# Optimization experiments

Hardware: AMD Instinct MI355X
Metric: run time of the kernel (lower is better)

Reference implementation:

```python
import jax, jax.numpy as jnp
import numpy as np

G = 8          # GroupNorm groups
EPS = 1e-5
L = 4          # num_layers
C = 64         # hidden_channels
CIN = 2        # in_channels


def group_norm(x, gamma, beta):
    B, Cc, H, W = x.shape
    xr = x.reshape(B, G, Cc // G, H, W)
    mu = xr.mean(axis=(2, 3, 4), keepdims=True)
    var = xr.var(axis=(2, 3, 4), keepdims=True)
    xn = ((xr - mu) * jax.lax.rsqrt(var + EPS)).reshape(B, Cc, H, W)
    return xn * gamma[:, None, None] + beta[:, None, None]


def conv1x1(x, w, b):
    # x: [B,Ci,H,W], w: [Co,Ci] -> [B,Co,H,W]
    return jnp.einsum('bchw,oc->bohw', x, w) + b[None, :, None, None]


def conv3x3(x, w, b):
    y = jax.lax.conv_general_dilated(x, w, (1, 1), 'SAME',
                                     dimension_numbers=('NCHW', 'OIHW', 'NCHW'))
    return y + b[None, :, None, None]


def setup_inputs() -> dict:
    key = jax.random.key(0)
    ks = jax.random.split(key, 20)
    s = 0.05
    inp = {
        'x': jax.random.normal(ks[0], (2, CIN, 256, 256), jnp.float32),
        'hidden': jnp.zeros((2, L, C, C), jnp.float32),
        'W_in': jax.random.normal(ks[1], (C, CIN, 3, 3), jnp.float32) * s,
        'b_in': jnp.zeros((C,), jnp.float32),
        'gamma': jnp.ones((L, C), jnp.float32),
        'beta': jnp.zeros((L, C), jnp.float32),
        'Wq': jax.random.normal(ks[2], (L, C, C), jnp.float32) * s,
        'bq': jnp.zeros((L, C), jnp.float32),
        'Wk': jax.random.normal(ks[3], (L, C, C), jnp.float32) * s,
        'bk': jnp.zeros((L, C), jnp.float32),
        'Wv': jax.random.normal(ks[4], (L, C, C), jnp.float32) * s,
        'bv': jnp.zeros((L, C), jnp.float32),
        'Wg': jax.random.normal(ks[5], (L, 2 * C, C), jnp.float32) * s,
        'bg': jnp.zeros((L, 2 * C), jnp.float32),
        'Wp': jax.random.normal(ks[6], (L, C, C), jnp.float32) * s,
        'bp': jnp.zeros((L, C), jnp.float32),
        'W_out': jax.random.normal(ks[7], (CIN, C, 3, 3), jnp.float32) * s,
        'b_out': jnp.zeros((CIN,), jnp.float32),
    }
    return inp


def gla_layer(feat, prev_mem, gamma, beta, Wq, bq, Wk, bk, Wv, bv, Wg, bg, Wp, bp):
    B, Cc, H, W = feat.shape
    N = H * W
    scale = Cc ** (-0.5)
    xn = group_norm(feat, gamma, beta)
    q = conv1x1(xn, Wq, bq).reshape(B, Cc, N) * scale
    k = conv1x1(xn, Wk, bk).reshape(B, Cc, N)
    v = conv1x1(xn, Wv, bv).reshape(B, Cc, N)
    gates = conv1x1(xn, Wg, bg).reshape(B, 2 * Cc, N)
    f_gate = jax.nn.sigmoid(gates[:, :Cc])
    i_gate = jax.nn.sigmoid(gates[:, Cc:])
    k_gated = k * i_gate
    new_knowledge = jnp.einsum('bcn,bdn->bcd', k_gated, v) / N  # [B,C,C]
    global_forget = f_gate.mean(axis=2)[:, :, None]              # [B,C,1]
    new_mem = global_forget * prev_mem + new_knowledge
    retrieved = jnp.einsum('bcn,bcd->bdn', q, new_mem).reshape(B, Cc, H, W)
    out = conv1x1(retrieved, Wp, bp) + feat
    return out, new_mem


def reference(x, hidden, W_in, b_in, gamma, beta, Wq, bq, Wk, bk, Wv, bv,
              Wg, bg, Wp, bp, W_out, b_out):
    feat = conv3x3(x, W_in, b_in)
    mems = []
    for i in range(L):
        feat, m = gla_layer(feat, hidden[:, i], gamma[i], beta[i],
                            Wq[i], bq[i], Wk[i], bk[i], Wv[i], bv[i],
                            Wg[i], bg[i], Wp[i], bp[i])
        mems.append(m)
    new_hidden = jnp.stack(mems, axis=1)  # [B,L,C,C]
    out = conv3x3(feat, W_out, b_out) + x
    return out, new_hidden
```

## Files before the change

kernel.cpp:

```cpp
#include <hip/hip_runtime.h>
#include <hip/hip_bf16.h>

typedef __hip_bfloat16 bf16;
typedef __attribute__((ext_vector_type(8))) short bf16x8;
typedef __attribute__((ext_vector_type(4))) short short4v;
typedef __attribute__((ext_vector_type(4))) float f32x4;

#define BATCH 2
#define CH 64
#define NPIX 65536
#define HDIM 256
#define NLAYER 4
#define NGRP 8
#define NSLOT 512

#define OFS_FEAT   0ull
#define OFS_KSLOT  16777216ull
#define OFS_MEMBG  25165824ull
#define OFS_FSUM   25182208ull
#define OFS_SSUM   25198592ull
#define OFS_BEFF   25214976ull
#define OFS_MEFFB  25215488ull
#define OFS_WKB    25231872ull
#define OFS_WVB    25264640ull
#define OFS_WGB    25297408ull
#define OFS_WTOUT  25362944ull
#define OFS_WPB    25367552ull
#define OFS_WQTB   25400320ull
#define ZERO_BYTES 32768

__device__ __forceinline__ float sigmoidf_(float x){ return 1.0f/(1.0f+__expf(-x)); }

__device__ __forceinline__ short f2bs(float x){
  unsigned u = __float_as_uint(x);
  u += 0x7fffu + ((u >> 16) & 1u);
  return (short)(u >> 16);
}
__device__ __forceinline__ float bs2f(short x){
  return __uint_as_float(((unsigned)(unsigned short)x) << 16);
}

__device__ __forceinline__ float waveReduce(float v){
  #pragma unroll
  for (int off=32; off; off>>=1) v += __shfl_xor(v, off, 64);
  return v;
}

__global__ void k_prepw(const float* __restrict__ Wk, const float* __restrict__ Wv,
                        const float* __restrict__ Wg, const float* __restrict__ Wout,
                        const float* __restrict__ Wp, const float* __restrict__ Wq,
                        short* __restrict__ Wkb, short* __restrict__ Wvb,
                        short* __restrict__ Wgb, float* __restrict__ wtout,
                        short* __restrict__ Wpb, short* __restrict__ Wqtb){
  int i = blockIdx.x*256 + threadIdx.x;
  if (i < 16384){
    Wkb[i] = f2bs(Wk[i]);
    Wvb[i] = f2bs(Wv[i]);
    Wpb[i] = f2bs(Wp[i]);
    int l = i >> 12, within = i & 4095;
    int e = within >> 6, c = within & 63;
    Wqtb[i] = f2bs(Wq[l*4096 + c*64 + e]);
  }
  if (i < 32768) Wgb[i] = f2bs(Wg[i]);
  if (i < 1152){
    int o = i / 576, rem = i % 576;
    int k = rem >> 6, c = rem & 63;
    wtout[(o*9 + k)*64 + c] = Wout[o*576 + c*9 + k];
  }
}

__device__ __forceinline__ void blockStats(const float* gs, const float* gq,
                                           float* ssum_b, int t){
  __shared__ float sacc[16];
  if (t < 16) sacc[t] = 0.f;
  __syncthreads();
  #pragma unroll
  for (int g=0; g<NGRP; g++){
    float s  = waveReduce(gs[g]);
    float sq = waveReduce(gq[g]);
    if ((t & 63) == 0){ atomicAdd(&sacc[g*2], s); atomicAdd(&sacc[g*2+1], sq); }
  }
  __syncthreads();
  if (t < 16) atomicAdd(&ssum_b[t*32], sacc[t]);
}

__global__ void k_conv_in(const float* __restrict__ x, const float* __restrict__ w,
                          const float* __restrict__ bias,
                          short* __restrict__ feat, float* __restrict__ ssum){
  int b = blockIdx.y;
  int t = threadIdx.x;
  int n = blockIdx.x*256 + t;
  int y = n >> 8, xx = n & 255;
  float patch[18];
  int idx = 0;
  #pragma unroll
  for (int ci=0; ci<2; ci++)
    #pragma unroll
    for (int dy=-1; dy<=1; dy++)
      #pragma unroll
      for (int dx=-1; dx<=1; dx++){
        int yy = y+dy, xc = xx+dx;
        float v = 0.f;
        if (yy>=0 && yy<HDIM && xc>=0 && xc<HDIM)
          v = x[((b*2+ci)*HDIM + yy)*HDIM + xc];
        patch[idx++] = v;
      }
  float gs[NGRP], gq[NGRP];
  #pragma unroll
  for (int g=0; g<NGRP; g++){ gs[g]=0.f; gq[g]=0.f; }
  short* fb = feat + ((size_t)b*NPIX + n)*64;
  #pragma unroll
  for (int c4=0; c4<16; c4++){
    short4v sv;
    #pragma unroll
    for (int j=0;j<4;j++){
      int o = c4*4 + j;
      float acc = bias[o];
      #pragma unroll
      for (int k=0; k<18; k++) acc += w[o*18+k]*patch[k];
      sv[j] = f2bs(acc);
      gs[o>>3] += acc; gq[o>>3] += acc*acc;
    }
    *(short4v*)(fb + c4*4) = sv;
  }
  blockStats(gs, gq, ssum + b*512, t);
}

__device__ __forceinline__ void gnCoef(const float* __restrict__ ssum_l, int b, int t,
                                       const float* __restrict__ gammaP,
                                       const float* __restrict__ betaP, int l,
                                       float* s_gnA, float* s_gnB){
  if (t < 64){
    int g = t >> 3;
    const float inv = 1.0f/(8.0f*NPIX);
    float s  = ssum_l[(b*16 + g*2)*32];
    float sq = ssum_l[(b*16 + g*2 + 1)*32];
    float mu = s*inv;
    float var = sq*inv - mu*mu;
    float rstd = rsqrtf(var + 1e-5f);
    float A = rstd * gammaP[l*64 + t];
    s_gnA[t] = A;
    s_gnB[t] = betaP[l*64 + t] - mu * A;
  }
}

__global__ __launch_bounds__(256,3) void k_qkvg_know(
    const short* __restrict__ feat, const float* __restrict__ ssum_l,
    const float* __restrict__ gammaP, const float* __restrict__ betaP,
    const short* __restrict__ Wkb, const float* __restrict__ bkP,
    const short* __restrict__ Wvb, const float* __restrict__ bvP,
    const short* __restrict__ Wgb, const float* __restrict__ bgP,
    int l, short* __restrict__ kslot, float* __restrict__ f_sum)
{
  int b = blockIdx.y;
  int n0 = blockIdx.x * 128;
  int t = threadIdx.x;
  int w = t >> 6;
  int lane = t & 63;
  int m = lane & 15;
  int quad = lane >> 4;
  int rowbase = w*16;

  __shared__ short s_buf[17408];
  short* s_kg = s_buf;
  short* s_v  = s_buf + 8704;
  short* s_xn = s_buf;
  __shared__ float s_gnA[64], s_gnB[64];

  gnCoef(ssum_l, b, t, gammaP, betaP, l, s_gnA, s_gnB);

  float bkv[4], biv[4], bvv[4], bfv[4], fs[4];
  #pragma unroll
  for (int r=0;r<4;r++){
    int row = rowbase + quad*4 + r;
    bkv[r] = bkP[l*64 + row];
    biv[r] = bgP[l*128 + 64 + row];
    bvv[r] = bvP[l*64 + row];
    bfv[r] = bgP[l*128 + row];
    fs[r] = 0.f;
  }
  f32x4 z4 = {0.f,0.f,0.f,0.f};
  f32x4 accn[4];
  #pragma unroll
  for (int dt=0;dt<4;dt++) accn[dt] = z4;

  __syncthreads();

  const short* fbase = feat + ((size_t)b*NPIX + n0)*64;
  #pragma unroll
  for (int i=0;i<4;i++){
    int chunk = t + i*256;
    int px = chunk >> 3, c8 = (chunk & 7)*8;
    bf16x8 rv = *(const bf16x8*)(fbase + px*64 + c8);
    short4v lo, hi;
    #pragma unroll
    for (int j=0;j<4;j++)
      lo[j] = f2bs(fmaf(bs2f(rv[j]), s_gnA[c8+j], s_gnB[c8+j]));
    #pragma unroll
    for (int j=0;j<4;j++)
      hi[j] = f2bs(fmaf(bs2f(rv[j+4]), s_gnA[c8+4+j], s_gnB[c8+4+j]));
    *(short4v*)&s_xn[px*72 + c8]     = lo;
    *(short4v*)&s_xn[px*72 + c8 + 4] = hi;
  }
  __syncthreads();

  bf16x8 Bf[2][8];
  #pragma unroll
  for (int kc=0;kc<2;kc++)
    #pragma unroll
    for (int nt=0;nt<8;nt++)
      Bf[kc][nt] = *(const bf16x8*)&s_xn[(nt*16+m)*72 + kc*32 + quad*8];
  __syncthreads();

  {
    bf16x8 Ak[2], Ai[2];
    #pragma unroll
    for (int kc=0;kc<2;kc++){
      Ak[kc] = *(const bf16x8*)&Wkb[l*4096 + (rowbase+m)*64 + kc*32 + quad*8];
      Ai[kc] = *(const bf16x8*)&Wgb[l*8192 + (64+rowbase+m)*64 + kc*32 + quad*8];
    }
    #pragma unroll
    for (int half=0; half<2; half++){
      f32x4 acck[4], acci[4];
      #pragma unroll
      for (int q4=0;q4<4;q4++){ acck[q4]=z4; acci[q4]=z4; }
      #pragma unroll
      for (int kc=0;kc<2;kc++)
        #pragma unroll
        for (int q4=0;q4<4;q4++){
          acck[q4] = __builtin_amdgcn_mfma_f32_16x16x32_bf16(Ak[kc], Bf[kc][half*4+q4], acck[q4], 0,0,0);
          acci[q4] = __builtin_amdgcn_mfma_f32_16x16x32_bf16(Ai[kc], Bf[kc][half*4+q4], acci[q4], 0,0,0);
        }
      #pragma unroll
      for (int q4=0;q4<4;q4++){
        int nt = half*4+q4;
        #pragma unroll
        for (int r=0;r<4;r++){
          int row = rowbase + quad*4 + r;
          float kv = acck[q4][r] + bkv[r];
          float iv = acci[q4][r] + biv[r];
          s_kg[row*136 + nt*16 + m] = f2bs(kv * sigmoidf_(iv));
        }
      }
    }
  }
  {
    bf16x8 Av[2];
    #pragma unroll
    for (int kc=0;kc<2;kc++)
      Av[kc] = *(const bf16x8*)&Wvb[l*4096 + (rowbase+m)*64 + kc*32 + quad*8];
    #pragma unroll
    for (int half=0; half<2; half++){
      f32x4 accv[4];
      #pragma unroll
      for (int q4=0;q4<4;q4++) accv[q4]=z4;
      #pragma unroll
      for (int kc=0;kc<2;kc++)
        #pragma unroll
        for (int q4=0;q4<4;q4++)
          accv[q4] = __builtin_amdgcn_mfma_f32_16x16x32_bf16(Av[kc], Bf[kc][half*4+q4], accv[q4], 0,0,0);
      #pragma unroll
      for (int q4=0;q4<4;q4++){
        int nt = half*4+q4;
        #pragma unroll
        for (int r=0;r<4;r++){
          int row = rowbase + quad*4 + r;
          s_v[row*136 + nt*16 + m] = f2bs(accv[q4][r] + bvv[r]);
        }
      }
    }
  }
  {
    bf16x8 Af[2];
    #pragma unroll
    for (int kc=0;kc<2;kc++)
      Af[kc] = *(const bf16x8*)&Wgb[l*8192 + (rowbase+m)*64 + kc*32 + quad*8];
    #pragma unroll
    for (int half=0; half<2; half++){
      f32x4 accf[4];
      #pragma unroll
      for (int q4=0;q4<4;q4++) accf[q4]=z4;
      #pragma unroll
      for (int kc=0;kc<2;kc++)
        #pragma unroll
        for (int q4=0;q4<4;q4++)
          accf[q4] = __builtin_amdgcn_mfma_f32_16x16x32_bf16(Af[kc], Bf[kc][half*4+q4], accf[q4], 0,0,0);
      #pragma unroll
      for (int q4=0;q4<4;q4++)
        #pragma unroll
        for (int r=0;r<4;r++)
          fs[r] += sigmoidf_(accf[q4][r] + bfv[r]);
    }
  }
  __syncthreads();

  #pragma unroll
  for (int kc4=0; kc4<4; kc4++){
    bf16x8 a = *(const bf16x8*)&s_kg[(rowbase + m)*136 + kc4*32 + quad*8];
    #pragma unroll
    for (int dt=0; dt<4; dt++){
      bf16x8 bv8 = *(const bf16x8*)&s_v[(dt*16 + m)*136 + kc4*32 + quad*8];
      accn[dt] = __builtin_amdgcn_mfma_f32_16x16x32_bf16(a, bv8, accn[dt], 0,0,0);
    }
  }

  #pragma unroll
  for (int off=1; off<16; off<<=1)
    #pragma unroll
    for (int r=0;r<4;r++) fs[r] += __shfl_xor(fs[r], off, 64);
  if (m == 0){
    #pragma unroll
    for (int r=0;r<4;r++)
      atomicAdd(&f_sum[(b*64 + rowbase + quad*4 + r)*32], fs[r]);
  }
  short* kr = kslot + ((size_t)b*NSLOT + blockIdx.x)*4096;
  #pragma unroll
  for (int dt=0;dt<4;dt++)
    #pragma unroll
    for (int r=0;r<4;r++)
      kr[(rowbase + quad*4 + r)*64 + dt*16 + m] = f2bs(accn[dt][r]);
}

__global__ __launch_bounds__(256) void k_memreduce(
    const short* __restrict__ kslot, const float* __restrict__ f_sum,
    const float* __restrict__ hidden_in, int l,
    float* __restrict__ hidden_out, short* __restrict__ membG)
{
  int b = blockIdx.y;
  int t = threadIdx.x;
  int e = t & 127;
  int half = t >> 7;
  int cd = blockIdx.x*128 + e;

  const short* base = kslot + ((size_t)b*NSLOT + half*256)*4096 + cd;
  float s = 0.f;
  #pragma unroll 16
  for (int sl=0; sl<256; sl++) s += bs2f(base[(size_t)sl*4096]);

  __shared__ float red[128];
  if (half) red[e] = s;
  __syncthreads();
  if (!half){
    const float invN = 1.0f/(float)NPIX;
    float kn = (s + red[e]) * invN;
    float fmean = f_sum[(b*64 + (cd>>6))*32] * invN;
    float pm = hidden_in[(size_t)(b*NLAYER+l)*4096 + cd];
    float nm = fmean*pm + kn;
    hidden_out[(size_t)(b*NLAYER+l)*4096 + cd] = nm;
    membG[b*4096 + cd] = f2bs(nm);
  }
}

__global__ __launch_bounds__(256) void k_meff(
    const short* __restrict__ membG, float* __restrict__ f_sum,
    const short* __restrict__ Wpb, const short* __restrict__ Wqtb,
    const float* __restrict__ bqP, const float* __restrict__ bpP,
    int l, short* __restrict__ Meffb, float* __restrict__ beff,
    float* __restrict__ ssum_next)
{
  int b = blockIdx.x;
  int t = threadIdx.x;
  int w = t >> 6;
  int lane = t & 63;
  int m = lane & 15;
  int quad = lane >> 4;

  __shared__ short s_memb[64*72];
  __shared__ short s_mfb[64*72];
  __shared__ float s_bq[64];

  if (t < 64) s_bq[t] = bqP[l*64 + t];

  #pragma unroll
  for (int i=0;i<16;i++){
    int cd = t + i*256;
    int c = cd >> 6, d = cd & 63;
    s_memb[c*72 + d] = membG[b*4096 + cd];
  }
  __syncthreads();
  if (t < 64) f_sum[(b*64 + t)*32] = 0.f;
  if (t < 16) ssum_next[(b*16 + t)*32] = 0.f;

  f32x4 z4 = {0.f,0.f,0.f,0.f};

  bf16x8 Ap[2];
  #pragma unroll
  for (int kc=0;kc<2;kc++)
    Ap[kc] = *(const bf16x8*)&Wpb[l*4096 + (w*16+m)*64 + kc*32 + quad*8];

  float be[4];
  #pragma unroll
  for (int r=0;r<4;r++) be[r] = 0.f;

  #pragma unroll
  for (int ct=0; ct<4; ct++){
    f32x4 a = z4;
    #pragma unroll
    for (int kc=0;kc<2;kc++){
      bf16x8 Bm = *(const bf16x8*)&s_memb[(ct*16+m)*72 + kc*32 + quad*8];
      a = __builtin_amdgcn_mfma_f32_16x16x32_bf16(Ap[kc], Bm, a, 0,0,0);
    }
    int c = ct*16 + m;
    #pragma unroll
    for (int r=0;r<4;r++){
      int o = w*16 + quad*4 + r;
      s_mfb[o*72 + c] = f2bs(a[r]);
      be[r] += a[r] * s_bq[c];
    }
  }
  #pragma unroll
  for (int off=1; off<16; off<<=1)
    #pragma unroll
    for (int r=0;r<4;r++) be[r] += __shfl_xor(be[r], off, 64);
  if (m == 0){
    #pragma unroll
    for (int r=0;r<4;r++){
      int o = w*16 + quad*4 + r;
      beff[b*64 + o] = bpP[l*64 + o] + 0.125f*be[r];
    }
  }
  __syncthreads();

  bf16x8 Am2[2];
  #pragma unroll
  for (int kc=0;kc<2;kc++)
    Am2[kc] = *(const bf16x8*)&s_mfb[(w*16+m)*72 + kc*32 + quad*8];
  #pragma unroll
  for (int et=0; et<4; et++){
    f32x4 a = z4;
    #pragma unroll
    for (int kc=0;kc<2;kc++){
      bf16x8 Bq = *(const bf16x8*)&Wqtb[l*4096 + (et*16+m)*64 + kc*32 + quad*8];
      a = __builtin_amdgcn_mfma_f32_16x16x32_bf16(Am2[kc], Bq, a, 0,0,0);
    }
    #pragma unroll
    for (int r=0;r<4;r++){
      int o = w*16 + quad*4 + r;
      Meffb[(size_t)b*4096 + o*64 + et*16 + m] = f2bs(0.125f*a[r]);
    }
  }
}

__global__ __launch_bounds__(256,3) void k_retrproj(
    const float* __restrict__ ssum_l,
    const float* __restrict__ gammaP, const float* __restrict__ betaP,
    const short* __restrict__ Meffb, const float* __restrict__ beff,
    int l, short* __restrict__ feat, float* __restrict__ ssum_next)
{
  int b = blockIdx.y;
  int n0 = blockIdx.x * 128;
  int t = threadIdx.x;
  int w = t >> 6;
  int lane = t & 63;
  int m = lane & 15;
  int quad = lane >> 4;

  __shared__ float s_out[128*68];
  short* s_xn = (short*)s_out;
  __shared__ float s_gnA[64], s_gnB[64], s_beff[64];
  __shared__ float s_sacc[16];

  gnCoef(ssum_l, b, t, gammaP, betaP, l, s_gnA, s_gnB);
  if (t < 64) s_beff[t] = beff[b*64 + t];
  if (t < 16) s_sacc[t] = 0.f;
  __syncthreads();

  short* fbase = feat + ((size_t)b*NPIX + n0)*64;
  #pragma unroll
  for (int i=0;i<4;i++){
    int chunk = t + i*256;
    int px = chunk >> 3, c8 = (chunk & 7)*8;
    bf16x8 rv = *(const bf16x8*)(fbase + px*64 + c8);
    short4v lo, hi;
    #pragma unroll
    for (int j=0;j<4;j++)
      lo[j] = f2bs(fmaf(bs2f(rv[j]), s_gnA[c8+j], s_gnB[c8+j]));
    #pragma unroll
    for (int j=0;j<4;j++)
      hi[j] = f2bs(fmaf(bs2f(rv[j+4]), s_gnA[c8+4+j], s_gnB[c8+4+j]));
    *(short4v*)&s_xn[px*72 + c8]     = lo;
    *(short4v*)&s_xn[px*72 + c8 + 4] = hi;
  }
  __syncthreads();

  bf16x8 Bf[2][8];
  #pragma unroll
  for (int kc=0;kc<2;kc++)
    #pragma unroll
    for (int nt=0;nt<8;nt++)
      Bf[kc][nt] = *(const bf16x8*)&s_xn[(nt*16+m)*72 + kc*32 + quad*8];

  bf16x8 Am[2];
  #pragma unroll
  for (int kc=0;kc<2;kc++)
    Am[kc] = *(const bf16x8*)&Meffb[(size_t)b*4096 + (w*16 + m)*64 + kc*32 + quad*8];
  __syncthreads();

  f32x4 acc[8];
  f32x4 z4 = {0.f,0.f,0.f,0.f};
  #pragma unroll
  for (int nt=0;nt<8;nt++) acc[nt]=z4;
  #pragma unroll
  for (int kc=0;kc<2;kc++)
    #pragma unroll
    for (int nt=0;nt<8;nt++)
      acc[nt] = __builtin_amdgcn_mfma_f32_16x16x32_bf16(Am[kc], Bf[kc][nt], acc[nt], 0,0,0);

  #pragma unroll
  for (int nt=0;nt<8;nt++)
    #pragma unroll
    for (int r=0;r<4;r++)
      s_out[(nt*16+m)*68 + w*16 + quad*4 + r] = acc[nt][r];
  __syncthreads();

  float gsv = 0.f, gqv = 0.f;
  int c8 = (t & 7)*8;
  #pragma unroll
  for (int i=0;i<4;i++){
    int chunk = t + i*256;
    int px = chunk >> 3;
    short* fp = fbase + px*64 + c8;
    bf16x8 rv = *(const bf16x8*)fp;
    f32x4 o1 = *(const f32x4*)&s_out[px*68 + c8];
    f32x4 o2 = *(const f32x4*)&s_out[px*68 + c8 + 4];
    short4v r1, r2;
    #pragma unroll
    for (int j=0;j<4;j++){
      float o = bs2f(rv[j]) + o1[j] + s_beff[c8+j];
      r1[j] = f2bs(o);
      gsv += o; gqv += o*o;
    }
    #pragma unroll
    for (int j=0;j<4;j++){
      float o = bs2f(rv[j+4]) + o2[j] + s_beff[c8+4+j];
      r2[j] = f2bs(o);
      gsv += o; gqv += o*o;
    }
    *(short4v*)fp = r1;
    *(short4v*)(fp+4) = r2;
  }
  gsv += __shfl_xor(gsv, 8, 64);  gqv += __shfl_xor(gqv, 8, 64);
  gsv += __shfl_xor(gsv, 16, 64); gqv += __shfl_xor(gqv, 16, 64);
  gsv += __shfl_xor(gsv, 32, 64); gqv += __shfl_xor(gqv, 32, 64);
  if ((lane & 56) == 0){
    int g = lane & 7;
    atomicAdd(&s_sacc[g*2], gsv);
    atomicAdd(&s_sacc[g*2+1], gqv);
  }
  __syncthreads();
  if (t < 16) atomicAdd(&ssum_next[(b*16 + t)*32], s_sacc[t]);
}

__global__ void k_conv_out(const short* __restrict__ feat, const float* __restrict__ wt,
                           const float* __restrict__ bias,
                           const float* __restrict__ xin, float* __restrict__ out){
  int b = blockIdx.y;
  int y = blockIdx.x;
  int xx = threadIdx.x;
  float acc0 = bias[0], acc1 = bias[1];
  #pragma unroll
  for (int dy=-1; dy<=1; dy++){
    int yy = y + dy;
    if (yy < 0 || yy >= HDIM) continue;
    #pragma unroll
    for (int dx=-1; dx<=1; dx++){
      int xc = xx + dx;
      if (xc >= 0 && xc < HDIM){
        const short* fp = feat + ((size_t)b*NPIX + yy*HDIM + xc)*64;
        const float* w0 = wt + ((0*3 + dy+1)*3 + dx+1)*64;
        const float* w1 = wt + ((1*3 + dy+1)*3 + dx+1)*64;
        #pragma unroll
        for (int c8=0;c8<8;c8++){
          bf16x8 fv = *(const bf16x8*)(fp + c8*8);
          f32x4 w0a = *(const f32x4*)(w0 + c8*8);
          f32x4 w0b = *(const f32x4*)(w0 + c8*8 + 4);
          f32x4 w1a = *(const f32x4*)(w1 + c8*8);
          f32x4 w1b = *(const f32x4*)(w1 + c8*8 + 4);
          #pragma unroll
          for (int j=0;j<4;j++){
            float fa = bs2f(fv[j]), fb2 = bs2f(fv[j+4]);
            acc0 += fa*w0a[j] + fb2*w0b[j];
            acc1 += fa*w1a[j] + fb2*w1b[j];
          }
        }
      }
    }
  }
  size_t p0 = (size_t)(b*2+0)*NPIX + y*HDIM + xx;
  size_t p1 = (size_t)(b*2+1)*NPIX + y*HDIM + xx;
  out[p0] = acc0 + xin[p0];
  out[p1] = acc1 + xin[p1];
}

extern "C" void kernel_launch(void* const* d_in, const int* in_sizes, int n_in,
                              void* d_out, int out_size, void* d_ws, size_t ws_size,
                              hipStream_t stream){
  char* ws = (char*)d_ws;
  short* feat  = (short*)(ws + OFS_FEAT);
  short* kslot = (short*)(ws + OFS_KSLOT);
  short* membg = (short*)(ws + OFS_MEMBG);
  float* fsum  = (float*)(ws + OFS_FSUM);
  float* ssum  = (float*)(ws + OFS_SSUM);
  float* beff  = (float*)(ws + OFS_BEFF);
  short* meffb = (short*)(ws + OFS_MEFFB);
  short* wkb   = (short*)(ws + OFS_WKB);
  short* wvb   = (short*)(ws + OFS_WVB);
  short* wgb   = (short*)(ws + OFS_WGB);
  float* wtout = (float*)(ws + OFS_WTOUT);
  short* wpb   = (short*)(ws + OFS_WPB);
  short* wqtb  = (short*)(ws + OFS_WQTB);

  const float* x      = (const float*)d_in[0];
  const float* hidden = (const float*)d_in[1];
  const float* W_in   = (const float*)d_in[2];
  const float* b_in   = (const float*)d_in[3];
  const float* gamma  = (const float*)d_in[4];
  const float* beta   = (const float*)d_in[5];
  const float* Wq     = (const float*)d_in[6];
  const float* bq     = (const float*)d_in[7];
  const float* Wk     = (const float*)d_in[8];
  const float* bk     = (const float*)d_in[9];
  const float* Wv     = (const float*)d_in[10];
  const float* bv     = (const float*)d_in[11];
  const float* Wg     = (const float*)d_in[12];
  const float* bg     = (const float*)d_in[13];
  const float* Wp     = (const float*)d_in[14];
  const float* bp     = (const float*)d_in[15];
  const float* W_out  = (const float*)d_in[16];
  const float* b_out  = (const float*)d_in[17];

  float* out        = (float*)d_out;
  float* hidden_out = out + BATCH*2*NPIX;

  hipMemsetAsync(ws + OFS_FSUM, 0, ZERO_BYTES, stream);
  k_prepw<<<dim3(128), dim3(256), 0, stream>>>(Wk, Wv, Wg, W_out, Wp, Wq,
                                               wkb, wvb, wgb, wtout, wpb, wqtb);
  k_conv_in<<<dim3(HDIM, BATCH), dim3(256), 0, stream>>>(x, W_in, b_in, feat, ssum);

  for (int l=0; l<NLAYER; l++){
    float* ssum_l = ssum + (l & 1)*1024;
    float* ssum_n = ssum + ((l+1) & 1)*1024;
    k_qkvg_know<<<dim3(NPIX/128, BATCH), dim3(256), 0, stream>>>(
        feat, ssum_l, gamma, beta, wkb, bk, wvb, bv, wgb, bg, l, kslot, fsum);
    k_memreduce<<<dim3(32, BATCH), dim3(256), 0, stream>>>(
        kslot, fsum, hidden, l, hidden_out, membg);
    k_meff<<<dim3(BATCH), dim3(256), 0, stream>>>(
        membg, fsum, wpb, wqtb, bq, bp, l, meffb, beff, ssum_n);
    k_retrproj<<<dim3(NPIX/128, BATCH), dim3(256), 0, stream>>>(
        ssum_l, gamma, beta, meffb, beff, l, feat, ssum_n);
  }

  k_conv_out<<<dim3(HDIM, BATCH), dim3(256), 0, stream>>>(feat, wtout, b_out, x, out);
}
```

Before: 358.1 us.

## Prefetch feature tiles early, raise MFMA priority, vectorize slot reduction

The two per-pixel kernels now issue their global loads of the feature tile before computing the GroupNorm coefficients and the first barrier, so load latency overlaps that setup work. MFMA sections are wrapped in s_setprio to favour matrix issue across waves. The memory-reduce kernel now has each thread read 8 contiguous bf16 values with a vector load and split the slots across 16 thread groups, followed by a shared-memory tree sum. This adds register pressure from holding the prefetched tiles.

```diff
diff --git a/kernel.cpp b/kernel.cpp
--- a/kernel.cpp
+++ b/kernel.cpp
@@ -167,6 +167,14 @@
   short* s_xn = s_buf;
   __shared__ float s_gnA[64], s_gnB[64];
 
+  const short* fbase = feat + ((size_t)b*NPIX + n0)*64;
+  bf16x8 rv[4];
+  #pragma unroll
+  for (int i=0;i<4;i++){
+    int chunk = t + i*256;
+    rv[i] = *(const bf16x8*)(fbase + (chunk >> 3)*64 + (chunk & 7)*8);
+  }
+
   gnCoef(ssum_l, b, t, gammaP, betaP, l, s_gnA, s_gnB);
 
   float bkv[4], biv[4], bvv[4], bfv[4], fs[4];
@@ -186,19 +194,17 @@
 
   __syncthreads();
 
-  const short* fbase = feat + ((size_t)b*NPIX + n0)*64;
   #pragma unroll
   for (int i=0;i<4;i++){
     int chunk = t + i*256;
     int px = chunk >> 3, c8 = (chunk & 7)*8;
-    bf16x8 rv = *(const bf16x8*)(fbase + px*64 + c8);
     short4v lo, hi;
     #pragma unroll
     for (int j=0;j<4;j++)
-      lo[j] = f2bs(fmaf(bs2f(rv[j]), s_gnA[c8+j], s_gnB[c8+j]));
+      lo[j] = f2bs(fmaf(bs2f(rv[i][j]), s_gnA[c8+j], s_gnB[c8+j]));
     #pragma unroll
     for (int j=0;j<4;j++)
-      hi[j] = f2bs(fmaf(bs2f(rv[j+4]), s_gnA[c8+4+j], s_gnB[c8+4+j]));
+      hi[j] = f2bs(fmaf(bs2f(rv[i][j+4]), s_gnA[c8+4+j], s_gnB[c8+4+j]));
     *(short4v*)&s_xn[px*72 + c8]     = lo;
     *(short4v*)&s_xn[px*72 + c8 + 4] = hi;
   }
@@ -224,6 +230,7 @@
       f32x4 acck[4], acci[4];
       #pragma unroll
       for (int q4=0;q4<4;q4++){ acck[q4]=z4; acci[q4]=z4; }
+      __builtin_amdgcn_s_setprio(1);
       #pragma unroll
       for (int kc=0;kc<2;kc++)
         #pragma unroll
@@ -231,6 +238,7 @@
           acck[q4] = __builtin_amdgcn_mfma_f32_16x16x32_bf16(Ak[kc], Bf[kc][half*4+q4], acck[q4], 0,0,0);
           acci[q4] = __builtin_amdgcn_mfma_f32_16x16x32_bf16(Ai[kc], Bf[kc][half*4+q4], acci[q4], 0,0,0);
         }
+      __builtin_amdgcn_s_setprio(0);
       #pragma unroll
       for (int q4=0;q4<4;q4++){
         int nt = half*4+q4;
@@ -254,11 +262,13 @@
       f32x4 accv[4];
       #pragma unroll
       for (int q4=0;q4<4;q4++) accv[q4]=z4;
+      __builtin_amdgcn_s_setprio(1);
       #pragma unroll
       for (int kc=0;kc<2;kc++)
         #pragma unroll
         for (int q4=0;q4<4;q4++)
           accv[q4] = __builtin_amdgcn_mfma_f32_16x16x32_bf16(Av[kc], Bf[kc][half*4+q4], accv[q4], 0,0,0);
+      __builtin_amdgcn_s_setprio(0);
       #pragma unroll
       for (int q4=0;q4<4;q4++){
         int nt = half*4+q4;
@@ -280,11 +290,13 @@
       f32x4 accf[4];
       #pragma unroll
       for (int q4=0;q4<4;q4++) accf[q4]=z4;
+      __builtin_amdgcn_s_setprio(1);
       #pragma unroll
       for (int kc=0;kc<2;kc++)
         #pragma unroll
         for (int q4=0;q4<4;q4++)
           accf[q4] = __builtin_amdgcn_mfma_f32_16x16x32_bf16(Af[kc], Bf[kc][half*4+q4], accf[q4], 0,0,0);
+      __builtin_amdgcn_s_setprio(0);
       #pragma unroll
       for (int q4=0;q4<4;q4++)
         #pragma unroll
@@ -294,6 +306,7 @@
   }
   __syncthreads();
 
+  __builtin_amdgcn_s_setprio(1);
   #pragma unroll
   for (int kc4=0; kc4<4; kc4++){
     bf16x8 a = *(const bf16x8*)&s_kg[(rowbase + m)*136 + kc4*32 + quad*8];
@@ -303,6 +316,7 @@
       accn[dt] = __builtin_amdgcn_mfma_f32_16x16x32_bf16(a, bv8, accn[dt], 0,0,0);
     }
   }
+  __builtin_amdgcn_s_setprio(0);
 
   #pragma unroll
   for (int off=1; off<16; off<<=1)
@@ -328,24 +342,35 @@
 {
   int b = blockIdx.y;
   int t = threadIdx.x;
-  int e = t & 127;
-  int half = t >> 7;
-  int cd = blockIdx.x*128 + e;
-
-  const short* base = kslot + ((size_t)b*NSLOT + half*256)*4096 + cd;
-  float s = 0.f;
-  #pragma unroll 16
-  for (int sl=0; sl<256; sl++) s += bs2f(base[(size_t)sl*4096]);
-
-  __shared__ float red[128];
-  if (half) red[e] = s;
-  __syncthreads();
-  if (!half){
+  int oct = t & 15;
+  int sg  = t >> 4;
+  int cd0 = blockIdx.x*128 + oct*8;
+
+  const short* base = kslot + ((size_t)b*NSLOT + sg*32)*4096 + cd0;
+  float s[8];
+  #pragma unroll
+  for (int j=0;j<8;j++) s[j]=0.f;
+  #pragma unroll 4
+  for (int sl=0; sl<32; sl++){
+    bf16x8 v = *(const bf16x8*)(base + (size_t)sl*4096);
+    #pragma unroll
+    for (int j=0;j<8;j++) s[j] += bs2f(v[j]);
+  }
+
+  __shared__ float red[16][128];
+  #pragma unroll
+  for (int j=0;j<8;j++) red[sg][oct*8+j] = s[j];
+  __syncthreads();
+
+  if (t < 128){
+    float tot = 0.f;
+    #pragma unroll
+    for (int g=0; g<16; g++) tot += red[g][t];
     const float invN = 1.0f/(float)NPIX;
-    float kn = (s + red[e]) * invN;
+    int cd = blockIdx.x*128 + t;
     float fmean = f_sum[(b*64 + (cd>>6))*32] * invN;
     float pm = hidden_in[(size_t)(b*NLAYER+l)*4096 + cd];
-    float nm = fmean*pm + kn;
+    float nm = fmean*pm + tot*invN;
     hidden_out[(size_t)(b*NLAYER+l)*4096 + cd] = nm;
     membG[b*4096 + cd] = f2bs(nm);
   }
@@ -460,24 +485,36 @@
   __shared__ float s_gnA[64], s_gnB[64], s_beff[64];
   __shared__ float s_sacc[16];
 
+  short* fbase = feat + ((size_t)b*NPIX + n0)*64;
+  bf16x8 rv[4];
+  #pragma unroll
+  for (int i=0;i<4;i++){
+    int chunk = t + i*256;
+    rv[i] = *(const bf16x8*)(fbase + (chunk >> 3)*64 + (chunk & 7)*8);
+  }
+
   gnCoef(ssum_l, b, t, gammaP, betaP, l, s_gnA, s_gnB);
   if (t < 64) s_beff[t] = beff[b*64 + t];
   if (t < 16) s_sacc[t] = 0.f;
-  __syncthreads();
-
-  short* fbase = feat + ((size_t)b*NPIX + n0)*64;
+
+  bf16x8 Am[2];
+  #pragma unroll
+  for (int kc=0;kc<2;kc++)
+    Am[kc] = *(const bf16x8*)&Meffb[(size_t)b*4096 + (w*16 + m)*64 + kc*32 + quad*8];
+
+  __syncthreads();
+
   #pragma unroll
   for (int i=0;i<4;i++){
     int chunk = t + i*256;
     int px = chunk >> 3, c8 = (chunk & 7)*8;
-    bf16x8 rv = *(const bf16x8*)(fbase + px*64 + c8);
     short4v lo, hi;
     #pragma unroll
     for (int j=0;j<4;j++)
-      lo[j] = f2bs(fmaf(bs2f(rv[j]), s_gnA[c8+j], s_gnB[c8+j]));
+      lo[j] = f2bs(fmaf(bs2f(rv[i][j]), s_gnA[c8+j], s_gnB[c8+j]));
     #pragma unroll
     for (int j=0;j<4;j++)
-      hi[j] = f2bs(fmaf(bs2f(rv[j+4]), s_gnA[c8+4+j], s_gnB[c8+4+j]));
+      hi[j] = f2bs(fmaf(bs2f(rv[i][j+4]), s_gnA[c8+4+j], s_gnB[c8+4+j]));
     *(short4v*)&s_xn[px*72 + c8]     = lo;
     *(short4v*)&s_xn[px*72 + c8 + 4] = hi;
   }
@@ -489,22 +526,19 @@
     #pragma unroll
     for (int nt=0;nt<8;nt++)
       Bf[kc][nt] = *(const bf16x8*)&s_xn[(nt*16+m)*72 + kc*32 + quad*8];
-
-  bf16x8 Am[2];
-  #pragma unroll
-  for (int kc=0;kc<2;kc++)
-    Am[kc] = *(const bf16x8*)&Meffb[(size_t)b*4096 + (w*16 + m)*64 + kc*32 + quad*8];
   __syncthreads();
 
   f32x4 acc[8];
   f32x4 z4 = {0.f,0.f,0.f,0.f};
   #pragma unroll
   for (int nt=0;nt<8;nt++) acc[nt]=z4;
+  __builtin_amdgcn_s_setprio(1);
   #pragma unroll
   for (int kc=0;kc<2;kc++)
     #pragma unroll
     for (int nt=0;nt<8;nt++)
       acc[nt] = __builtin_amdgcn_mfma_f32_16x16x32_bf16(Am[kc], Bf[kc][nt], acc[nt], 0,0,0);
+  __builtin_amdgcn_s_setprio(0);
 
   #pragma unroll
   for (int nt=0;nt<8;nt++)
@@ -520,19 +554,19 @@
     int chunk = t + i*256;
     int px = chunk >> 3;
     short* fp = fbase + px*64 + c8;
-    bf16x8 rv = *(const bf16x8*)fp;
+    bf16x8 rv2 = *(const bf16x8*)fp;
     f32x4 o1 = *(const f32x4*)&s_out[px*68 + c8];
     f32x4 o2 = *(const f32x4*)&s_out[px*68 + c8 + 4];
     short4v r1, r2;
     #pragma unroll
     for (int j=0;j<4;j++){
-      float o = bs2f(rv[j]) + o1[j] + s_beff[c8+j];
+      float o = bs2f(rv2[j]) + o1[j] + s_beff[c8+j];
       r1[j] = f2bs(o);
       gsv += o; gqv += o*o;
     }
     #pragma unroll
     for (int j=0;j<4;j++){
-      float o = bs2f(rv[j+4]) + o2[j] + s_beff[c8+4+j];
+      float o = bs2f(rv2[j+4]) + o2[j] + s_beff[c8+4+j];
       r2[j] = f2bs(o);
       gsv += o; gqv += o*o;
     }
```

Measured after the change: 340.0 us. 5.1% less time.
